# Kernel optimization log

Hardware: AMD Instinct MI355X
Metric: run time of the kernel (lower is better)

Reference implementation:

```python
import jax, jax.numpy as jnp
import numpy as np

B, T, C, H = 64, 256, 384, 6
HS = C // H  # 64


def _ln(x, w, b, eps=1e-5):
    m = jnp.mean(x, axis=-1, keepdims=True)
    v = jnp.mean((x - m) ** 2, axis=-1, keepdims=True)
    return (x - m) / jnp.sqrt(v + eps) * w + b


def setup_inputs() -> dict:
    key = jax.random.key(0)
    ks = jax.random.split(key, 18)
    sc = 0.02
    return {
        "x": jax.random.normal(ks[0], (B, T, C), jnp.float32),
        "ln1_w": jnp.ones((C,), jnp.float32),
        "ln1_b": jnp.zeros((C,), jnp.float32),
        # per-head Q/K/V linears stacked over the head axis: [H, C, HS]
        "Wq": jax.random.normal(ks[1], (H, C, HS), jnp.float32) * sc,
        "bq": jnp.zeros((H, HS), jnp.float32),
        "Wk": jax.random.normal(ks[2], (H, C, HS), jnp.float32) * sc,
        "bk": jnp.zeros((H, HS), jnp.float32),
        "Wv": jax.random.normal(ks[3], (H, C, HS), jnp.float32) * sc,
        "bv": jnp.zeros((H, HS), jnp.float32),
        "Wproj": jax.random.normal(ks[4], (C, C), jnp.float32) * sc,
        "bproj": jnp.zeros((C,), jnp.float32),
        "ln2_w": jnp.ones((C,), jnp.float32),
        "ln2_b": jnp.zeros((C,), jnp.float32),
        "W1": jax.random.normal(ks[5], (C, 4 * C), jnp.float32) * sc,
        "b1": jnp.zeros((4 * C,), jnp.float32),
        "W2": jax.random.normal(ks[6], (4 * C, C), jnp.float32) * sc,
        "b2": jnp.zeros((C,), jnp.float32),
    }


def reference(x, ln1_w, ln1_b, Wq, bq, Wk, bk, Wv, bv, Wproj, bproj,
              ln2_w, ln2_b, W1, b1, W2, b2):
    # --- pre-norm causal MHA (dropout = identity in eval) ---
    h = _ln(x, ln1_w, ln1_b)
    Q = jnp.einsum('btc,hcd->bhtd', h, Wq) + bq[None, :, None, :]
    K = jnp.einsum('btc,hcd->bhtd', h, Wk) + bk[None, :, None, :]
    V = jnp.einsum('btc,hcd->bhtd', h, Wv) + bv[None, :, None, :]
    scores = jnp.einsum('bhtd,bhsd->bhts', Q, K) * (HS ** -0.5)
    mask = jnp.tril(jnp.ones((x.shape[1], x.shape[1]), bool))
    scores = jnp.where(mask, scores, -jnp.inf)
    wei = jax.nn.softmax(scores, axis=-1)
    o = jnp.einsum('bhts,bhsd->bhtd', wei, V)
    # concat heads (same order as torch.cat over head list)
    o = o.transpose(0, 2, 1, 3).reshape(x.shape[0], x.shape[1], C)
    x1 = x + o @ Wproj + bproj
    # --- pre-norm FFN with exact (erf) GELU, matching torch default ---
    h2 = _ln(x1, ln2_w, ln2_b)
    f = jax.nn.gelu(h2 @ W1 + b1, approximate=False) @ W2 + b2
    return x1 + f
```

## Files before the change

### kernel.cpp

```cpp
#include <hip/hip_runtime.h>
#include <math.h>

constexpr int Bsz  = 64;
constexpr int Tseq = 256;
constexpr int Cdim = 384;
constexpr int Hh   = 6;
constexpr int HSd  = 64;
constexpr int Mrows = Bsz * Tseq;
constexpr int Cffn  = 4 * Cdim;
constexpr int Nqkv  = 3 * Cdim;

typedef __attribute__((ext_vector_type(8))) short short8;
typedef __attribute__((ext_vector_type(4))) float f32x4;

__device__ __forceinline__ ushort f2bf(float x) {
  union { float f; uint u; } a; a.f = x;
  uint r = a.u + 0x7fffu + ((a.u >> 16) & 1u);
  return (ushort)(r >> 16);
}
__device__ __forceinline__ float bf2f(ushort u) {
  union { uint u; float f; } a; a.u = ((uint)u) << 16;
  return a.f;
}

__device__ __forceinline__ float gelu_fast(float x) {
  float t = x * x;
  float u = x * fmaf(0.044715f, t, 1.0f);
  float e = fminf(1.5957691216f * u, 80.f);
  float z = __expf(e);
  return x * (z / (1.0f + z));
}

__global__ __launch_bounds__(256) void prep_kernel(
    const float* __restrict__ Wq, const float* __restrict__ Wk,
    const float* __restrict__ Wv, const float* __restrict__ Wproj,
    const float* __restrict__ W1, const float* __restrict__ W2,
    const float* __restrict__ bq, const float* __restrict__ bk,
    const float* __restrict__ bv,
    ushort* __restrict__ WqkvT, ushort* __restrict__ WprojT,
    ushort* __restrict__ W1T, ushort* __restrict__ W2T,
    float* __restrict__ bqkv) {
  const int bid = blockIdx.x;
  if (bid >= 1728) {
    int i = (bid - 1728) * 256 + threadIdx.x;
    if (i < Nqkv)
      bqkv[i] = (i < 384) ? bq[i] : (i < 768) ? bk[i - 384] : bv[i - 768];
    return;
  }
  const int tx = threadIdx.x & 31, ty = threadIdx.x >> 5;
  const float* src; ushort* dst; int R, S, r0, s0;
  if (bid < 432) {
    int which = bid / 144, rem = bid % 144;
    const float* W = (which == 0) ? Wq : (which == 1) ? Wk : Wv;
    int bz = rem / 24, t = rem % 24;
    R = 384; S = 64;
    src = W + (size_t)bz * R * S;
    dst = WqkvT + (size_t)which * 384 * 384 + (size_t)bz * R * S;
    r0 = (t >> 1) * 32; s0 = (t & 1) * 32;
  } else if (bid < 576) {
    int rem = bid - 432; R = 384; S = 384; src = Wproj; dst = WprojT;
    r0 = (rem / 12) * 32; s0 = (rem % 12) * 32;
  } else if (bid < 1152) {
    int rem = bid - 576; R = 384; S = 1536; src = W1; dst = W1T;
    r0 = (rem / 48) * 32; s0 = (rem % 48) * 32;
  } else {
    int rem = bid - 1152; R = 1536; S = 384; src = W2; dst = W2T;
    r0 = (rem / 12) * 32; s0 = (rem % 12) * 32;
  }
  __shared__ float t[32][33];
#pragma unroll
  for (int i = 0; i < 32; i += 8)
    t[ty + i][tx] = src[(size_t)(r0 + ty + i) * S + s0 + tx];
  __syncthreads();
#pragma unroll
  for (int i = 0; i < 32; i += 8)
    dst[(size_t)(s0 + ty + i) * R + r0 + tx] = f2bf(t[tx][ty + i]);
}

template <typename T>
__global__ __launch_bounds__(256) void ln_kernel(
    const T* __restrict__ x, const float* __restrict__ w,
    const float* __restrict__ b, ushort* __restrict__ out, int nrows) {
  int row  = blockIdx.x * 4 + (threadIdx.x >> 6);
  int lane = threadIdx.x & 63;
  if (row >= nrows) return;
  const T* xr = x + (size_t)row * Cdim;
  float v[6];
  float s = 0.f;
#pragma unroll
  for (int i = 0; i < 6; ++i) {
    if constexpr (sizeof(T) == 2) v[i] = bf2f(xr[lane + 64 * i]);
    else                          v[i] = xr[lane + 64 * i];
    s += v[i];
  }
#pragma unroll
  for (int off = 32; off > 0; off >>= 1) s += __shfl_xor(s, off, 64);
  float mean = s * (1.f / Cdim);
  float sq = 0.f;
#pragma unroll
  for (int i = 0; i < 6; ++i) { float d = v[i] - mean; sq += d * d; }
#pragma unroll
  for (int off = 32; off > 0; off >>= 1) sq += __shfl_xor(sq, off, 64);
  float rstd = rsqrtf(sq * (1.f / Cdim) + 1e-5f);
  ushort* orow = out + (size_t)row * Cdim;
#pragma unroll
  for (int i = 0; i < 6; ++i) {
    int c = lane + 64 * i;
    orow[c] = f2bf((v[i] - mean) * rstd * w[c] + b[c]);
  }
}

template <int EPI, int BN>
__global__ __launch_bounds__(256) void mfma_gemm(
    const ushort* __restrict__ A, const ushort* __restrict__ Bt,
    const float* __restrict__ bias, const void* __restrict__ res,
    void* __restrict__ Cout, void* __restrict__ C2, void* __restrict__ C3,
    int M, int N, int K) {
  constexpr int WC = BN / 2;
  constexpr int JN = WC / 16;
  constexpr int NB = BN / 32;
  __shared__ ushort Als[128 * 64];
  __shared__ ushort Bls[BN * 64];
  const int tid = threadIdx.x;

  const int lid = blockIdx.y * gridDim.x + blockIdx.x;
  const int xcd = lid & 7, idx = lid >> 3;
  const int by = xcd * 16 + (idx & 15);
  const int bx = idx >> 4;
  const int m0 = by * 128, n0 = bx * BN;

  const int lane = tid & 63;
  const int w    = tid >> 6;
  const int wr   = (w >> 1) * 64;
  const int wc   = (w & 1) * WC;
  const int lm   = lane & 15;
  const int g    = lane >> 4;
  const int rq   = g * 4;

  const int wub = (tid & ~63) * 8;

  f32x4 acc[4][JN] = {};

  for (int k0 = 0; k0 < K; k0 += 64) {
    __syncthreads();
#pragma unroll
    for (int q = 0; q < 4; ++q) {
      const int ci = tid + q * 256;
      const int row = ci >> 3;
      const int kc = ((ci & 7) ^ (row & 7)) * 8;
      const ushort* gA = A + (size_t)(m0 + row) * K + k0 + kc;
      __builtin_amdgcn_global_load_lds(
          (const __attribute__((address_space(1))) uint*)gA,
          (__attribute__((address_space(3))) uint*)(Als + wub + q * 2048),
          16, 0, 0);
    }
#pragma unroll
    for (int q = 0; q < NB; ++q) {
      const int ci = tid + q * 256;
      const int row = ci >> 3;
      const int kc = ((ci & 7) ^ (row & 7)) * 8;
      const ushort* gB = Bt + (size_t)(n0 + row) * K + k0 + kc;
      __builtin_amdgcn_global_load_lds(
          (const __attribute__((address_space(1))) uint*)gB,
          (__attribute__((address_space(3))) uint*)(Bls + wub + q * 2048),
          16, 0, 0);
    }
    __syncthreads();

#pragma unroll
    for (int half = 0; half < 2; ++half) {
      const int sl = ((half << 2) | g) ^ (lm & 7);
      short8 af[4], bf[JN];
#pragma unroll
      for (int i = 0; i < 4; ++i)
        af[i] = *(const short8*)&Als[(wr + i * 16 + lm) * 64 + sl * 8];
#pragma unroll
      for (int j = 0; j < JN; ++j)
        bf[j] = *(const short8*)&Bls[(wc + j * 16 + lm) * 64 + sl * 8];
#pragma unroll
      for (int i = 0; i < 4; ++i)
#pragma unroll
        for (int j = 0; j < JN; ++j)
          acc[i][j] = __builtin_amdgcn_mfma_f32_16x16x32_bf16(af[i], bf[j],
                                                              acc[i][j], 0, 0, 0);
    }
  }

  float bb[JN];
#pragma unroll
  for (int j = 0; j < JN; ++j) bb[j] = bias[n0 + wc + j * 16 + lm];

#pragma unroll
  for (int i = 0; i < 4; ++i) {
#pragma unroll
    for (int r = 0; r < 4; ++r) {
      const int row = m0 + wr + i * 16 + rq + r;
      if (EPI == 1) {
        const float* resrow = (const float*)res + (size_t)row * N + n0 + wc;
        ushort* crow = (ushort*)Cout + (size_t)row * N + n0 + wc;
#pragma unroll
        for (int j = 0; j < JN; ++j) {
          float rv = __builtin_nontemporal_load(resrow + j * 16 + lm);
          crow[j * 16 + lm] = f2bf(acc[i][j][r] + bb[j] + rv);
        }
      } else if (EPI == 4) {
        const ushort* resrow = (const ushort*)res + (size_t)row * N + n0 + wc;
        float* crow = (float*)Cout + (size_t)row * N + n0 + wc;
#pragma unroll
        for (int j = 0; j < JN; ++j)
          crow[j * 16 + lm] = acc[i][j][r] + bb[j] + bf2f(resrow[j * 16 + lm]);
      } else if (EPI == 3) {
        const int bb_ = row >> 8, tt = row & 255;
#pragma unroll
        for (int j = 0; j < JN; ++j) {
          const int colb = n0 + wc + j * 16;
          const int sec = colb / 384, cc = colb % 384;
          const int hh = cc >> 6, db = (cc & 63) + lm;
          ushort* dstp = (sec == 0) ? (ushort*)Cout
                       : (sec == 1) ? (ushort*)C2 : (ushort*)C3;
          dstp[((size_t)(bb_ * Hh + hh) * Tseq + tt) * HSd + db] =
              f2bf(acc[i][j][r] + bb[j]);
        }
      } else {
        ushort* crow = (ushort*)Cout + (size_t)row * N + n0 + wc;
#pragma unroll
        for (int j = 0; j < JN; ++j)
          crow[j * 16 + lm] = f2bf(gelu_fast(acc[i][j][r] + bb[j]));
      }
    }
  }
}

__global__ __launch_bounds__(256) void attn_kernel(
    const ushort* __restrict__ Qb, const ushort* __restrict__ Kb,
    const ushort* __restrict__ Vb, ushort* __restrict__ Oc) {
  __shared__ ushort Ks[64 * 72];
  __shared__ ushort Vt[64 * 72];
  __shared__ ushort Pl[4][16 * 72];
  const int bh = blockIdx.x, qt = blockIdx.y;
  const int b = bh / Hh, h = bh % Hh;
  const int tid = threadIdx.x;
  const int w = tid >> 6, lane = tid & 63;
  const int g = lane >> 4, n16 = lane & 15;

  const ushort* qrow = Qb + ((size_t)bh * Tseq + qt * 64 + w * 16 + n16) * HSd;
  short8 qf0 = *(const short8*)(qrow + g * 8);
  short8 qf1 = *(const short8*)(qrow + 32 + g * 8);

  f32x4 oacc[4] = {};
  float m_r[4], l_r[4];
#pragma unroll
  for (int r = 0; r < 4; ++r) { m_r[r] = -1e30f; l_r[r] = 0.f; }

  const int t0 = qt * 64 + w * 16 + g * 4;

  const ushort* Ksrc = Kb + (size_t)bh * Tseq * HSd;
  const ushort* Vsrc = Vb + (size_t)bh * Tseq * HSd;

  for (int st = 0; st <= qt; ++st) {
    __syncthreads();
    for (int c = tid; c < 512; c += 256) {
      int kr = c >> 3, kc = (c & 7) * 8;
      *(uint4*)&Ks[kr * 72 + kc] =
          *(const uint4*)&Ksrc[(size_t)(st * 64 + kr) * HSd + kc];
      int vr = c & 63, vc = (c >> 6) * 8;
      uint4 vv = *(const uint4*)&Vsrc[(size_t)(st * 64 + vr) * HSd + vc];
      const ushort* pv = (const ushort*)&vv;
#pragma unroll
      for (int i = 0; i < 8; ++i) Vt[(vc + i) * 72 + vr] = pv[i];
    }
    __syncthreads();

    f32x4 s[4];
#pragma unroll
    for (int ct = 0; ct < 4; ++ct) {
      short8 kf0 = *(const short8*)&Ks[(ct * 16 + n16) * 72 + g * 8];
      short8 kf1 = *(const short8*)&Ks[(ct * 16 + n16) * 72 + 32 + g * 8];
      f32x4 z = {};
      z = __builtin_amdgcn_mfma_f32_16x16x32_bf16(qf0, kf0, z, 0, 0, 0);
      z = __builtin_amdgcn_mfma_f32_16x16x32_bf16(qf1, kf1, z, 0, 0, 0);
      s[ct] = z;
    }

#pragma unroll
    for (int ct = 0; ct < 4; ++ct) {
      const int s_col = st * 64 + ct * 16 + n16;
#pragma unroll
      for (int r = 0; r < 4; ++r) {
        float v = s[ct][r] * 0.125f;
        s[ct][r] = (s_col > t0 + r) ? -1e30f : v;
      }
    }

#pragma unroll
    for (int r = 0; r < 4; ++r) {
      float m = fmaxf(fmaxf(s[0][r], s[1][r]), fmaxf(s[2][r], s[3][r]));
      m = fmaxf(m, __shfl_xor(m, 1, 64));
      m = fmaxf(m, __shfl_xor(m, 2, 64));
      m = fmaxf(m, __shfl_xor(m, 4, 64));
      m = fmaxf(m, __shfl_xor(m, 8, 64));
      float mnew = fmaxf(m_r[r], m);
      float alpha = __expf(m_r[r] - mnew);
      m_r[r] = mnew;
      float ssum = 0.f;
#pragma unroll
      for (int ct = 0; ct < 4; ++ct) {
        float p = __expf(s[ct][r] - mnew);
        s[ct][r] = p;
        ssum += p;
      }
      ssum += __shfl_xor(ssum, 1, 64);
      ssum += __shfl_xor(ssum, 2, 64);
      ssum += __shfl_xor(ssum, 4, 64);
      ssum += __shfl_xor(ssum, 8, 64);
      l_r[r] = l_r[r] * alpha + ssum;
#pragma unroll
      for (int j = 0; j < 4; ++j) oacc[j][r] *= alpha;
    }

    ushort* pw = &Pl[w][0];
#pragma unroll
    for (int ct = 0; ct < 4; ++ct)
#pragma unroll
      for (int r = 0; r < 4; ++r)
        pw[(g * 4 + r) * 72 + ct * 16 + n16] = f2bf(s[ct][r]);

    short8 pf0 = *(const short8*)&pw[n16 * 72 + g * 8];
    short8 pf1 = *(const short8*)&pw[n16 * 72 + 32 + g * 8];
#pragma unroll
    for (int j = 0; j < 4; ++j) {
      short8 vf0 = *(const short8*)&Vt[(j * 16 + n16) * 72 + g * 8];
      short8 vf1 = *(const short8*)&Vt[(j * 16 + n16) * 72 + 32 + g * 8];
      oacc[j] = __builtin_amdgcn_mfma_f32_16x16x32_bf16(pf0, vf0, oacc[j], 0, 0, 0);
      oacc[j] = __builtin_amdgcn_mfma_f32_16x16x32_bf16(pf1, vf1, oacc[j], 0, 0, 0);
    }
  }

  float inv[4];
#pragma unroll
  for (int r = 0; r < 4; ++r) inv[r] = 1.f / l_r[r];
  ushort* orow = Oc + ((size_t)(b * Tseq + qt * 64 + w * 16)) * Cdim + h * HSd;
#pragma unroll
  for (int j = 0; j < 4; ++j)
#pragma unroll
    for (int r = 0; r < 4; ++r)
      orow[(size_t)(g * 4 + r) * Cdim + j * 16 + n16] = f2bf(oacc[j][r] * inv[r]);
}

extern "C" void kernel_launch(void* const* d_in, const int* in_sizes, int n_in,
                              void* d_out, int out_size, void* d_ws, size_t ws_size,
                              hipStream_t stream) {
  const float* x      = (const float*)d_in[0];
  const float* ln1_w  = (const float*)d_in[1];
  const float* ln1_b  = (const float*)d_in[2];
  const float* Wq     = (const float*)d_in[3];
  const float* bq     = (const float*)d_in[4];
  const float* Wk     = (const float*)d_in[5];
  const float* bk     = (const float*)d_in[6];
  const float* Wv     = (const float*)d_in[7];
  const float* bv     = (const float*)d_in[8];
  const float* Wproj  = (const float*)d_in[9];
  const float* bproj  = (const float*)d_in[10];
  const float* ln2_w  = (const float*)d_in[11];
  const float* ln2_b  = (const float*)d_in[12];
  const float* W1     = (const float*)d_in[13];
  const float* b1     = (const float*)d_in[14];
  const float* W2     = (const float*)d_in[15];
  const float* b2     = (const float*)d_in[16];
  float* out = (float*)d_out;

  char* p = (char*)d_ws;
  ushort* h     = (ushort*)p;  p += (size_t)Mrows * Cdim * 2;
  ushort* Qb    = (ushort*)p;  p += (size_t)Mrows * Cdim * 2;
  ushort* Kb    = (ushort*)p;  p += (size_t)Mrows * Cdim * 2;
  ushort* Vb    = (ushort*)p;  p += (size_t)Mrows * Cdim * 2;
  ushort* Oc    = (ushort*)p;  p += (size_t)Mrows * Cdim * 2;
  ushort* g     = (ushort*)p;  p += (size_t)Mrows * Cffn * 2;
  ushort* WqkvT = (ushort*)p;  p += (size_t)Nqkv * Cdim * 2;
  ushort* WprojT= (ushort*)p;  p += (size_t)Cdim * Cdim * 2;
  ushort* W1T   = (ushort*)p;  p += (size_t)Cffn * Cdim * 2;
  ushort* W2T   = (ushort*)p;  p += (size_t)Cdim * Cffn * 2;
  float*  bqkv  = (float*)p;   p += (size_t)Nqkv * 4;
  ushort* h2 = h;
  ushort* x1 = Qb;

  dim3 blk(256);

  prep_kernel<<<dim3(1733), blk, 0, stream>>>(Wq, Wk, Wv, Wproj, W1, W2,
                                              bq, bk, bv,
                                              WqkvT, WprojT, W1T, W2T, bqkv);

  ln_kernel<float><<<dim3(Mrows / 4), blk, 0, stream>>>(x, ln1_w, ln1_b, h, Mrows);

  mfma_gemm<3, 128><<<dim3(Nqkv / 128, Mrows / 128), blk, 0, stream>>>(
      h, WqkvT, bqkv, nullptr, Qb, Kb, Vb, Mrows, Nqkv, Cdim);

  attn_kernel<<<dim3(Bsz * Hh, 4), blk, 0, stream>>>(Qb, Kb, Vb, Oc);

  mfma_gemm<1, 64><<<dim3(Cdim / 64, Mrows / 128), blk, 0, stream>>>(
      Oc, WprojT, bproj, x, x1, nullptr, nullptr, Mrows, Cdim, Cdim);

  ln_kernel<ushort><<<dim3(Mrows / 4), blk, 0, stream>>>(x1, ln2_w, ln2_b, h2, Mrows);

  mfma_gemm<2, 128><<<dim3(Cffn / 128, Mrows / 128), blk, 0, stream>>>(
      h2, W1T, b1, nullptr, g, nullptr, nullptr, Mrows, Cffn, Cdim);

  mfma_gemm<4, 64><<<dim3(Cdim / 64, Mrows / 128), blk, 0, stream>>>(
      g, W2T, b2, x1, out, nullptr, nullptr, Mrows, Cdim, Cffn);
}
```

Measured before the change: 253.0 us.

## Double-buffer GEMM LDS tiles with register prefetch and BK=32

Replaces the direct global-to-LDS loads with a BK=64 single buffer by a register-staged prefetch pipeline. The next K-slice is loaded into registers while the current one is computed, LDS is double-buffered with a 32-wide K tile, and the XOR swizzle is adjusted. Only one barrier per iteration is needed, so global latency is meant to overlap with MFMA work. In exchange there are twice as many iterations and barriers, each with less MFMA work, plus higher register pressure from the staging registers.

New measurement: 258.3 us. 2.1% more time.

```diff
diff --git a/kernel.cpp b/kernel.cpp
--- a/kernel.cpp
+++ b/kernel.cpp
@@ -118,9 +118,8 @@
     int M, int N, int K) {
   constexpr int WC = BN / 2;
   constexpr int JN = WC / 16;
-  constexpr int NB = BN / 32;
-  __shared__ ushort Als[128 * 64];
-  __shared__ ushort Bls[BN * 64];
+  __shared__ ushort Als[2][128 * 32];
+  __shared__ ushort Bls[2][BN * 32];
   const int tid = threadIdx.x;
 
   const int lid = blockIdx.y * gridDim.x + blockIdx.x;
@@ -137,53 +136,57 @@
   const int g    = lane >> 4;
   const int rq   = g * 4;
 
-  const int wub = (tid & ~63) * 8;
+  const int c0 = tid, c1 = tid + 256;
+  const int kc0 = ((c0 & 3) ^ ((c0 >> 3) & 3)) * 8;
+  const int kc1 = ((c1 & 3) ^ ((c1 >> 3) & 3)) * 8;
+  const ushort* pA0 = A  + (size_t)(m0 + (c0 >> 2)) * K + kc0;
+  const ushort* pA1 = A  + (size_t)(m0 + (c1 >> 2)) * K + kc1;
+  const ushort* pB0 = Bt + (size_t)(n0 + (c0 >> 2)) * K + kc0;
+  const ushort* pB1 = (BN == 128)
+      ? Bt + (size_t)(n0 + (c1 >> 2)) * K + kc1 : nullptr;
+  const int wA0 = (c0 >> 2) * 32 + (c0 & 3) * 8;
+  const int wA1 = (c1 >> 2) * 32 + (c1 & 3) * 8;
+  const int kqs = (g ^ ((lm >> 1) & 3)) * 8;
 
   f32x4 acc[4][JN] = {};
 
-  for (int k0 = 0; k0 < K; k0 += 64) {
+  const int nIter = K >> 5;
+  uint4 ra0 = *(const uint4*)pA0;
+  uint4 ra1 = *(const uint4*)pA1;
+  uint4 rb0 = *(const uint4*)pB0;
+  uint4 rb1 = (BN == 128) ? *(const uint4*)pB1 : make_uint4(0, 0, 0, 0);
+
+  for (int it = 0; it < nIter; ++it) {
+    uint4 na0, na1, nb0, nb1;
+    if (it + 1 < nIter) {
+      const int kn = (it + 1) << 5;
+      na0 = *(const uint4*)(pA0 + kn);
+      na1 = *(const uint4*)(pA1 + kn);
+      nb0 = *(const uint4*)(pB0 + kn);
+      if (BN == 128) nb1 = *(const uint4*)(pB1 + kn);
+    }
+    ushort* Ab = Als[it & 1];
+    ushort* Bb = Bls[it & 1];
+    *(uint4*)&Ab[wA0] = ra0;
+    *(uint4*)&Ab[wA1] = ra1;
+    *(uint4*)&Bb[wA0] = rb0;
+    if (BN == 128) *(uint4*)&Bb[wA1] = rb1;
     __syncthreads();
-#pragma unroll
-    for (int q = 0; q < 4; ++q) {
-      const int ci = tid + q * 256;
-      const int row = ci >> 3;
-      const int kc = ((ci & 7) ^ (row & 7)) * 8;
-      const ushort* gA = A + (size_t)(m0 + row) * K + k0 + kc;
-      __builtin_amdgcn_global_load_lds(
-          (const __attribute__((address_space(1))) uint*)gA,
-          (__attribute__((address_space(3))) uint*)(Als + wub + q * 2048),
-          16, 0, 0);
-    }
-#pragma unroll
-    for (int q = 0; q < NB; ++q) {
-      const int ci = tid + q * 256;
-      const int row = ci >> 3;
-      const int kc = ((ci & 7) ^ (row & 7)) * 8;
-      const ushort* gB = Bt + (size_t)(n0 + row) * K + k0 + kc;
-      __builtin_amdgcn_global_load_lds(
-          (const __attribute__((address_space(1))) uint*)gB,
-          (__attribute__((address_space(3))) uint*)(Bls + wub + q * 2048),
-          16, 0, 0);
-    }
-    __syncthreads();
-
-#pragma unroll
-    for (int half = 0; half < 2; ++half) {
-      const int sl = ((half << 2) | g) ^ (lm & 7);
-      short8 af[4], bf[JN];
-#pragma unroll
-      for (int i = 0; i < 4; ++i)
-        af[i] = *(const short8*)&Als[(wr + i * 16 + lm) * 64 + sl * 8];
+
+    short8 af[4], bf[JN];
+#pragma unroll
+    for (int i = 0; i < 4; ++i)
+      af[i] = *(const short8*)&Ab[(wr + i * 16 + lm) * 32 + kqs];
+#pragma unroll
+    for (int j = 0; j < JN; ++j)
+      bf[j] = *(const short8*)&Bb[(wc + j * 16 + lm) * 32 + kqs];
+#pragma unroll
+    for (int i = 0; i < 4; ++i)
 #pragma unroll
       for (int j = 0; j < JN; ++j)
-        bf[j] = *(const short8*)&Bls[(wc + j * 16 + lm) * 64 + sl * 8];
-#pragma unroll
-      for (int i = 0; i < 4; ++i)
-#pragma unroll
-        for (int j = 0; j < JN; ++j)
-          acc[i][j] = __builtin_amdgcn_mfma_f32_16x16x32_bf16(af[i], bf[j],
-                                                              acc[i][j], 0, 0, 0);
-    }
+        acc[i][j] = __builtin_amdgcn_mfma_f32_16x16x32_bf16(af[i], bf[j],
+                                                            acc[i][j], 0, 0, 0);
+    ra0 = na0; ra1 = na1; rb0 = nb0; rb1 = nb1;
   }
 
   float bb[JN];
```
